# Kernel optimization log

Measured on AMD Instinct MI355X. Metric: run time of the kernel, lower is better.

The kernel has to match this reference:

```python
import jax, jax.numpy as jnp
import numpy as np

N_NODES = 50000
IN_DIM = 256
LATENT = 128
HIDDEN = 2 * LATENT  # 256


def _xavier(key, fan_in, fan_out):
    # matches nn.init.xavier_uniform_ on a [out, in] weight; we store as [in, out]
    limit = float(np.sqrt(6.0 / (fan_in + fan_out)))
    return jax.random.uniform(key, (fan_in, fan_out), jnp.float32, -limit, limit)


def setup_inputs() -> dict:
    key = jax.random.key(0)
    ks = jax.random.split(key, 8)
    x = jax.random.normal(ks[0], (N_NODES, IN_DIM), jnp.float32)
    edge_index = jax.random.randint(ks[1], (2, 800000), 0, N_NODES, jnp.int64)
    W1 = _xavier(ks[2], IN_DIM, HIDDEN)
    b1 = jnp.zeros((HIDDEN,), jnp.float32)
    Wmu = _xavier(ks[3], HIDDEN, LATENT)
    bmu = jnp.zeros((LATENT,), jnp.float32)
    Wlv = _xavier(ks[4], HIDDEN, LATENT)
    blv = jnp.zeros((LATENT,), jnp.float32)
    return {"x": x, "edge_index": edge_index, "W1": W1, "b1": b1,
            "Wmu": Wmu, "bmu": bmu, "Wlv": Wlv, "blv": blv}


def _gcn_layer(x, W, b, src, dst):
    # PyG GCNConv: h = x @ W; add self loops; symmetric norm; scatter-add; + bias
    h = x @ W  # [N, out]
    ones = jnp.ones(src.shape[0], x.dtype)
    deg = jax.ops.segment_sum(ones, dst, num_segments=N_NODES) + 1.0  # +1 for self loop
    dinv = jax.lax.rsqrt(deg)  # deg >= 1 always
    norm = dinv[src] * dinv[dst]  # [E]
    agg = jax.ops.segment_sum(h[src] * norm[:, None], dst, num_segments=N_NODES)
    agg = agg + h * (dinv * dinv)[:, None]  # self-loop contribution, norm_ii = 1/deg_i
    return agg + b


def reference(x, edge_index, W1, b1, Wmu, bmu, Wlv, blv):
    src, dst = edge_index[0], edge_index[1]
    z = _gcn_layer(x, W1, b1, src, dst)
    z = jax.nn.relu(z)
    # dropout in eval mode == identity
    mu = _gcn_layer(z, Wmu, bmu, src, dst)
    logvar = _gcn_layer(z, Wlv, blv, src, dst)
    return (mu, logvar)
```

## Files before the change

### kernel.cpp

```cpp
#include <hip/hip_runtime.h>

#define N_NODES 50000
#define E_EDGES 800000
#define D 256
#define L 128
#define CAP 64

typedef __attribute__((ext_vector_type(8))) short bf16x8;
typedef __attribute__((ext_vector_type(4))) float f32x4;

__device__ __forceinline__ float bf2f(unsigned short u) {
    union { unsigned int i; float f; } v; v.i = ((unsigned int)u) << 16; return v.f;
}
__device__ __forceinline__ unsigned short f2bf(float f) {
    union { float f; unsigned int i; } v; v.f = f;
    unsigned int r = v.i + 0x7fffu + ((v.i >> 16) & 1u);
    return (unsigned short)(r >> 16);
}

__global__ __launch_bounds__(256) void fill_fixed(const int* __restrict__ src,
                                                  const int* __restrict__ dst,
                                                  int* __restrict__ cursor,
                                                  int* __restrict__ bucket) {
    int e = blockIdx.x * 256 + threadIdx.x;
    if (e >= E_EDGES) return;
    int d = dst[e];
    int pos = atomicAdd(&cursor[d], 1);
    if (pos < CAP) bucket[d * CAP + pos] = src[e];
}

__global__ __launch_bounds__(256) void dinv_fin(const int* __restrict__ cursor,
                                                float* __restrict__ dinv) {
    int i = blockIdx.x * 256 + threadIdx.x;
    if (i < N_NODES) dinv[i] = rsqrtf((float)cursor[i] + 1.0f);
}

__global__ __launch_bounds__(256) void setup(
    const float* __restrict__ W1, const float* __restrict__ Wmu,
    const float* __restrict__ Wlv, const float* __restrict__ bmu,
    const float* __restrict__ blv,
    unsigned short* __restrict__ W1h, unsigned short* __restrict__ W1l,
    unsigned short* __restrict__ Wch, unsigned short* __restrict__ Wcl,
    float* __restrict__ bcat, int* __restrict__ cursor) {
    int b = blockIdx.x, t = threadIdx.x;
    if (b < 256) {
        int n = b, k = t;
        float w = W1[k * 256 + n];
        unsigned short h = f2bf(w);
        W1h[n * 256 + k] = h;
        W1l[n * 256 + k] = f2bf(w - bf2f(h));
    } else if (b < 512) {
        int n = b - 256, k = t;
        float w = (n < 128) ? Wmu[k * 128 + n] : Wlv[k * 128 + (n - 128)];
        unsigned short h = f2bf(w);
        Wch[n * 256 + k] = h;
        Wcl[n * 256 + k] = f2bf(w - bf2f(h));
        if (b == 256) bcat[t] = (t < 128) ? bmu[t] : blv[t - 128];
    } else {
        int i = (b - 512) * 256 + t;
        if (i < N_NODES) cursor[i] = 0;
    }
}

__global__ __launch_bounds__(256, 2) void gemm_mfma(
    const float* __restrict__ A,
    const unsigned short* __restrict__ Bth, const unsigned short* __restrict__ Btl,
    unsigned short* __restrict__ Hout, int M)
{
    __shared__ unsigned short Ash[128 * 32];
    __shared__ unsigned short Asl[128 * 32];
    __shared__ unsigned short Bsh[256 * 32];
    __shared__ unsigned short Bsl[256 * 32];
    const int t = threadIdx.x;
    const int lane = t & 63, wave = t >> 6;
    const int m_ = lane & 15, q = lane >> 4;
    const int wr = wave >> 1, wc = wave & 1;
    const int row0 = blockIdx.x * 128;
    const int sr = t >> 2;
    const int sc = t & 3;

    f32x4 acc[4][8];
    const f32x4 zf = {0.f, 0.f, 0.f, 0.f};
#pragma unroll
    for (int rs = 0; rs < 4; ++rs)
#pragma unroll
        for (int nt = 0; nt < 8; ++nt) acc[rs][nt] = zf;

    for (int ks = 0; ks < 8; ++ks) {
        const int k0 = ks * 32;
        bf16x8 gbh[4], gbl[4];
#pragma unroll
        for (int i = 0; i < 4; ++i) {
            int n = sr + i * 64;
            gbh[i] = *(const bf16x8*)(Bth + n * 256 + k0 + sc * 8);
            gbl[i] = *(const bf16x8*)(Btl + n * 256 + k0 + sc * 8);
        }
        float4 ga0[2], ga1[2];
#pragma unroll
        for (int p = 0; p < 2; ++p) {
            int r = row0 + p * 64 + sr; if (r >= M) r = M - 1;
            const float* Xp = A + (size_t)r * 256 + k0 + sc * 8;
            ga0[p] = *(const float4*)Xp;
            ga1[p] = *(const float4*)(Xp + 4);
        }
        __syncthreads();
#pragma unroll
        for (int p = 0; p < 2; ++p) {
            int lr = p * 64 + sr;
            int cc = (sc ^ ((lr >> 1) & 3)) * 8;
            float af[8] = {ga0[p].x, ga0[p].y, ga0[p].z, ga0[p].w,
                           ga1[p].x, ga1[p].y, ga1[p].z, ga1[p].w};
            bf16x8 h, l;
#pragma unroll
            for (int j = 0; j < 8; ++j) {
                unsigned short hh = f2bf(af[j]);
                h[j] = (short)hh;
                l[j] = (short)f2bf(af[j] - bf2f(hh));
            }
            *(bf16x8*)&Ash[lr * 32 + cc] = h;
            *(bf16x8*)&Asl[lr * 32 + cc] = l;
        }
#pragma unroll
        for (int i = 0; i < 4; ++i) {
            int n = sr + i * 64;
            int cc = (sc ^ ((n >> 1) & 3)) * 8;
            *(bf16x8*)&Bsh[n * 32 + cc] = gbh[i];
            *(bf16x8*)&Bsl[n * 32 + cc] = gbl[i];
        }
        __syncthreads();
        bf16x8 ah[4], al[4];
#pragma unroll
        for (int rs = 0; rs < 4; ++rs) {
            int r = wr * 64 + rs * 16 + m_;
            int cc = (q ^ ((r >> 1) & 3)) * 8;
            ah[rs] = *(const bf16x8*)&Ash[r * 32 + cc];
            al[rs] = *(const bf16x8*)&Asl[r * 32 + cc];
        }
#pragma unroll
        for (int nt = 0; nt < 8; ++nt) {
            int n = wc * 128 + nt * 16 + m_;
            int cr = (q ^ ((n >> 1) & 3)) * 8;
            bf16x8 bh = *(const bf16x8*)&Bsh[n * 32 + cr];
            bf16x8 bl = *(const bf16x8*)&Bsl[n * 32 + cr];
#pragma unroll
            for (int rs = 0; rs < 4; ++rs) {
                acc[rs][nt] = __builtin_amdgcn_mfma_f32_16x16x32_bf16(ah[rs], bh, acc[rs][nt], 0, 0, 0);
                acc[rs][nt] = __builtin_amdgcn_mfma_f32_16x16x32_bf16(ah[rs], bl, acc[rs][nt], 0, 0, 0);
                acc[rs][nt] = __builtin_amdgcn_mfma_f32_16x16x32_bf16(al[rs], bh, acc[rs][nt], 0, 0, 0);
            }
        }
    }
#pragma unroll
    for (int rs = 0; rs < 4; ++rs) {
        int rbase = row0 + wr * 64 + rs * 16 + q * 4;
#pragma unroll
        for (int rr = 0; rr < 4; ++rr) {
            int grow = rbase + rr;
            if (grow >= M) continue;
#pragma unroll
            for (int nt = 0; nt < 8; ++nt) {
                int gcol = wc * 128 + nt * 16 + m_;
                Hout[(size_t)grow * 256 + gcol] = f2bf(acc[rs][nt][rr]);
            }
        }
    }
}

__global__ __launch_bounds__(256, 2) void gemm_bf16(
    const unsigned short* __restrict__ A,
    const unsigned short* __restrict__ Bth, const unsigned short* __restrict__ Btl,
    unsigned short* __restrict__ Tout, int M)
{
    __shared__ unsigned short Ash[128 * 32];
    __shared__ unsigned short Bsh[256 * 32];
    __shared__ unsigned short Bsl[256 * 32];
    const int t = threadIdx.x;
    const int lane = t & 63, wave = t >> 6;
    const int m_ = lane & 15, q = lane >> 4;
    const int wr = wave >> 1, wc = wave & 1;
    const int row0 = blockIdx.x * 128;
    const int sr = t >> 2;
    const int sc = t & 3;

    f32x4 acc[4][8];
    const f32x4 zf = {0.f, 0.f, 0.f, 0.f};
#pragma unroll
    for (int rs = 0; rs < 4; ++rs)
#pragma unroll
        for (int nt = 0; nt < 8; ++nt) acc[rs][nt] = zf;

    for (int ks = 0; ks < 8; ++ks) {
        const int k0 = ks * 32;
        bf16x8 gbh[4], gbl[4];
#pragma unroll
        for (int i = 0; i < 4; ++i) {
            int n = sr + i * 64;
            gbh[i] = *(const bf16x8*)(Bth + n * 256 + k0 + sc * 8);
            gbl[i] = *(const bf16x8*)(Btl + n * 256 + k0 + sc * 8);
        }
        bf16x8 gav[2];
#pragma unroll
        for (int p = 0; p < 2; ++p) {
            int r = row0 + p * 64 + sr; if (r >= M) r = M - 1;
            gav[p] = *(const bf16x8*)(A + (size_t)r * 256 + k0 + sc * 8);
        }
        __syncthreads();
#pragma unroll
        for (int p = 0; p < 2; ++p) {
            int lr = p * 64 + sr;
            int cc = (sc ^ ((lr >> 1) & 3)) * 8;
            *(bf16x8*)&Ash[lr * 32 + cc] = gav[p];
        }
#pragma unroll
        for (int i = 0; i < 4; ++i) {
            int n = sr + i * 64;
            int cc = (sc ^ ((n >> 1) & 3)) * 8;
            *(bf16x8*)&Bsh[n * 32 + cc] = gbh[i];
            *(bf16x8*)&Bsl[n * 32 + cc] = gbl[i];
        }
        __syncthreads();
        bf16x8 ah[4];
#pragma unroll
        for (int rs = 0; rs < 4; ++rs) {
            int r = wr * 64 + rs * 16 + m_;
            int cc = (q ^ ((r >> 1) & 3)) * 8;
            ah[rs] = *(const bf16x8*)&Ash[r * 32 + cc];
        }
#pragma unroll
        for (int nt = 0; nt < 8; ++nt) {
            int n = wc * 128 + nt * 16 + m_;
            int cr = (q ^ ((n >> 1) & 3)) * 8;
            bf16x8 bh = *(const bf16x8*)&Bsh[n * 32 + cr];
            bf16x8 bl = *(const bf16x8*)&Bsl[n * 32 + cr];
#pragma unroll
            for (int rs = 0; rs < 4; ++rs) {
                acc[rs][nt] = __builtin_amdgcn_mfma_f32_16x16x32_bf16(ah[rs], bh, acc[rs][nt], 0, 0, 0);
                acc[rs][nt] = __builtin_amdgcn_mfma_f32_16x16x32_bf16(ah[rs], bl, acc[rs][nt], 0, 0, 0);
            }
        }
    }
#pragma unroll
    for (int rs = 0; rs < 4; ++rs) {
        int rbase = row0 + wr * 64 + rs * 16 + q * 4;
#pragma unroll
        for (int rr = 0; rr < 4; ++rr) {
            int grow = rbase + rr;
            if (grow >= M) continue;
#pragma unroll
            for (int nt = 0; nt < 8; ++nt) {
                int gcol = wc * 128 + nt * 16 + m_;
                Tout[(size_t)grow * 256 + gcol] = f2bf(acc[rs][nt][rr]);
            }
        }
    }
}

__global__ __launch_bounds__(256) void gather_pre(
    const unsigned short* __restrict__ Hs,
    const int* __restrict__ bucket, const int* __restrict__ cnt_,
    const float* __restrict__ dinv, const float* __restrict__ bias,
    unsigned short* __restrict__ OutZ,
    float* __restrict__ mu, float* __restrict__ lv, int mode)
{
    const int lane = threadIdx.x & 63;
    const int hl = lane & 31;
    const int bb = lane & 32;
    const int node = blockIdx.x * 8 + (threadIdx.x >> 5);
    const int col = hl * 8;
    int cnt = cnt_[node]; if (cnt > CAP) cnt = CAP;
    float dn = dinv[node];

    int   s0r = 0, s1r = 0;
    float w0r = 0.f, w1r = 0.f;
    if (hl < cnt)      { s0r = bucket[node * CAP + hl];      w0r = dinv[s0r] * dn; }
    if (hl + 32 < cnt) { s1r = bucket[node * CAP + 32 + hl]; w1r = dinv[s1r] * dn; }

    float sl = dn * dn;
    bf16x8 hv = *(const bf16x8*)(Hs + (size_t)node * D + col);
    float a[8];
#pragma unroll
    for (int p = 0; p < 8; ++p) a[p] = bf2f((unsigned short)hv[p]) * sl;

    const int cnt0 = cnt < 32 ? cnt : 32;
    int j = 0;
    for (; j + 3 < cnt0; j += 4) {
        int t0 = __shfl(s0r, bb + j,     64), t1 = __shfl(s0r, bb + j + 1, 64);
        int t2 = __shfl(s0r, bb + j + 2, 64), t3 = __shfl(s0r, bb + j + 3, 64);
        float w0 = __shfl(w0r, bb + j,     64), w1 = __shfl(w0r, bb + j + 1, 64);
        float w2 = __shfl(w0r, bb + j + 2, 64), w3 = __shfl(w0r, bb + j + 3, 64);
        bf16x8 u0 = *(const bf16x8*)(Hs + (size_t)t0 * D + col);
        bf16x8 u1 = *(const bf16x8*)(Hs + (size_t)t1 * D + col);
        bf16x8 u2 = *(const bf16x8*)(Hs + (size_t)t2 * D + col);
        bf16x8 u3 = *(const bf16x8*)(Hs + (size_t)t3 * D + col);
#pragma unroll
        for (int p = 0; p < 8; ++p) a[p] = fmaf(bf2f((unsigned short)u0[p]), w0, a[p]);
#pragma unroll
        for (int p = 0; p < 8; ++p) a[p] = fmaf(bf2f((unsigned short)u1[p]), w1, a[p]);
#pragma unroll
        for (int p = 0; p < 8; ++p) a[p] = fmaf(bf2f((unsigned short)u2[p]), w2, a[p]);
#pragma unroll
        for (int p = 0; p < 8; ++p) a[p] = fmaf(bf2f((unsigned short)u3[p]), w3, a[p]);
    }
    for (; j < cnt0; ++j) {
        int   t0 = __shfl(s0r, bb + j, 64);
        float w0 = __shfl(w0r, bb + j, 64);
        bf16x8 u0 = *(const bf16x8*)(Hs + (size_t)t0 * D + col);
#pragma unroll
        for (int p = 0; p < 8; ++p) a[p] = fmaf(bf2f((unsigned short)u0[p]), w0, a[p]);
    }
    if (cnt > 32) {
        for (int j2 = 0; j2 < cnt - 32; ++j2) {
            int   t0 = __shfl(s1r, bb + j2, 64);
            float w0 = __shfl(w1r, bb + j2, 64);
            bf16x8 u0 = *(const bf16x8*)(Hs + (size_t)t0 * D + col);
#pragma unroll
            for (int p = 0; p < 8; ++p) a[p] = fmaf(bf2f((unsigned short)u0[p]), w0, a[p]);
        }
    }

    float4 b0 = *(const float4*)(bias + col);
    float4 b1 = *(const float4*)(bias + col + 4);
    float bf[8] = {b0.x, b0.y, b0.z, b0.w, b1.x, b1.y, b1.z, b1.w};
    if (mode == 0) {
        bf16x8 o;
#pragma unroll
        for (int p = 0; p < 8; ++p) o[p] = (short)f2bf(fmaxf(a[p] + bf[p], 0.f));
        *(bf16x8*)(OutZ + (size_t)node * D + col) = o;
    } else {
        float4 o0, o1;
        o0.x = a[0] + bf[0]; o0.y = a[1] + bf[1];
        o0.z = a[2] + bf[2]; o0.w = a[3] + bf[3];
        o1.x = a[4] + bf[4]; o1.y = a[5] + bf[5];
        o1.z = a[6] + bf[6]; o1.w = a[7] + bf[7];
        float* Op = (col < 128) ? (mu + (size_t)node * L + col)
                                : (lv + (size_t)node * L + (col - 128));
        *(float4*)Op = o0;
        *(float4*)(Op + 4) = o1;
    }
}

extern "C" void kernel_launch(void* const* d_in, const int* in_sizes, int n_in,
                              void* d_out, int out_size, void* d_ws, size_t ws_size,
                              hipStream_t stream) {
    const float* x   = (const float*)d_in[0];
    const int*   ei  = (const int*)d_in[1];
    const float* W1  = (const float*)d_in[2];
    const float* b1  = (const float*)d_in[3];
    const float* Wmu = (const float*)d_in[4];
    const float* bmu = (const float*)d_in[5];
    const float* Wlv = (const float*)d_in[6];
    const float* blv = (const float*)d_in[7];
    const int* src = ei;
    const int* dst = ei + E_EDGES;

    const size_t NF = (size_t)N_NODES * D;
    unsigned short* Hb = (unsigned short*)d_ws;
    unsigned short* Z  = Hb + NF;
    unsigned short* T  = Z + NF;
    unsigned short* W1h = T + NF;
    unsigned short* W1l = W1h + 65536;
    unsigned short* Wch = W1l + 65536;
    unsigned short* Wcl = Wch + 65536;
    float* bcat = (float*)(Wcl + 65536);
    float* dinv = bcat + 256;
    int* cursor = (int*)(dinv + N_NODES);
    int* bucket = cursor + N_NODES;
    float* mu = (float*)d_out;
    float* lv = mu + (size_t)N_NODES * L;

    setup<<<512 + (N_NODES + 255) / 256, 256, 0, stream>>>(
        W1, Wmu, Wlv, bmu, blv, W1h, W1l, Wch, Wcl, bcat, cursor);
    fill_fixed<<<(E_EDGES + 255) / 256, 256, 0, stream>>>(src, dst, cursor, bucket);
    dinv_fin<<<(N_NODES + 255) / 256, 256, 0, stream>>>(cursor, dinv);

    const int gemm_blocks = (N_NODES + 127) / 128;
    const int gat_blocks  = N_NODES / 8;
    gemm_mfma<<<gemm_blocks, 256, 0, stream>>>(x, W1h, W1l, Hb, N_NODES);
    gather_pre<<<gat_blocks, 256, 0, stream>>>(Hb, bucket, cursor, dinv, b1,
                                               Z, nullptr, nullptr, 0);
    gemm_bf16<<<gemm_blocks, 256, 0, stream>>>(Z, Wch, Wcl, T, N_NODES);
    gather_pre<<<gat_blocks, 256, 0, stream>>>(T, bucket, cursor, dinv, bcat,
                                               nullptr, mu, lv, 1);
}
```

Baseline: 315.2 us.

## Halve GEMM row tile, prefetch next K slice, compute dinv inline in gather

Both GEMM kernels now use 64-row tiles instead of 128, with fewer accumulators and a launch bound of 3 blocks per CU. They also register-prefetch the next K slice of A and B while the current slice runs on MFMA. The dinv_fin kernel and its buffer are removed, and gather_pre computes rsqrt of degree+1 from the cursor counts on the fly. The aim is higher occupancy, better overlap of global loads with compute, and one fewer launch. The cost is more reloading of B per row, redundant rsqrt work in the gathers, and extra register pressure from the prefetch buffers.

```diff
diff --git a/kernel.cpp b/kernel.cpp
--- a/kernel.cpp
+++ b/kernel.cpp
@@ -27,12 +27,6 @@
     int d = dst[e];
     int pos = atomicAdd(&cursor[d], 1);
     if (pos < CAP) bucket[d * CAP + pos] = src[e];
-}
-
-__global__ __launch_bounds__(256) void dinv_fin(const int* __restrict__ cursor,
-                                                float* __restrict__ dinv) {
-    int i = blockIdx.x * 256 + threadIdx.x;
-    if (i < N_NODES) dinv[i] = rsqrtf((float)cursor[i] + 1.0f);
 }
 
 __global__ __launch_bounds__(256) void setup(
@@ -62,54 +56,49 @@
     }
 }
 
-__global__ __launch_bounds__(256, 2) void gemm_mfma(
+__global__ __launch_bounds__(256, 3) void gemm_mfma(
     const float* __restrict__ A,
     const unsigned short* __restrict__ Bth, const unsigned short* __restrict__ Btl,
     unsigned short* __restrict__ Hout, int M)
 {
-    __shared__ unsigned short Ash[128 * 32];
-    __shared__ unsigned short Asl[128 * 32];
+    __shared__ unsigned short Ash[64 * 32];
+    __shared__ unsigned short Asl[64 * 32];
     __shared__ unsigned short Bsh[256 * 32];
     __shared__ unsigned short Bsl[256 * 32];
     const int t = threadIdx.x;
     const int lane = t & 63, wave = t >> 6;
     const int m_ = lane & 15, q = lane >> 4;
     const int wr = wave >> 1, wc = wave & 1;
-    const int row0 = blockIdx.x * 128;
+    const int row0 = blockIdx.x * 64;
     const int sr = t >> 2;
     const int sc = t & 3;
 
-    f32x4 acc[4][8];
+    int rA = row0 + sr; if (rA >= M) rA = M - 1;
+    const float* Ap = A + (size_t)rA * 256;
+
+    f32x4 acc[2][8];
     const f32x4 zf = {0.f, 0.f, 0.f, 0.f};
 #pragma unroll
-    for (int rs = 0; rs < 4; ++rs)
+    for (int rs = 0; rs < 2; ++rs)
 #pragma unroll
         for (int nt = 0; nt < 8; ++nt) acc[rs][nt] = zf;
 
+    bf16x8 gbh[4], gbl[4];
+    float4 ga0, ga1;
+#pragma unroll
+    for (int i = 0; i < 4; ++i) {
+        int n = sr + i * 64;
+        gbh[i] = *(const bf16x8*)(Bth + n * 256 + sc * 8);
+        gbl[i] = *(const bf16x8*)(Btl + n * 256 + sc * 8);
+    }
+    ga0 = *(const float4*)(Ap + sc * 8);
+    ga1 = *(const float4*)(Ap + sc * 8 + 4);
+
     for (int ks = 0; ks < 8; ++ks) {
-        const int k0 = ks * 32;
-        bf16x8 gbh[4], gbl[4];
-#pragma unroll
-        for (int i = 0; i < 4; ++i) {
-            int n = sr + i * 64;
-            gbh[i] = *(const bf16x8*)(Bth + n * 256 + k0 + sc * 8);
-            gbl[i] = *(const bf16x8*)(Btl + n * 256 + k0 + sc * 8);
-        }
-        float4 ga0[2], ga1[2];
-#pragma unroll
-        for (int p = 0; p < 2; ++p) {
-            int r = row0 + p * 64 + sr; if (r >= M) r = M - 1;
-            const float* Xp = A + (size_t)r * 256 + k0 + sc * 8;
-            ga0[p] = *(const float4*)Xp;
-            ga1[p] = *(const float4*)(Xp + 4);
-        }
         __syncthreads();
-#pragma unroll
-        for (int p = 0; p < 2; ++p) {
-            int lr = p * 64 + sr;
-            int cc = (sc ^ ((lr >> 1) & 3)) * 8;
-            float af[8] = {ga0[p].x, ga0[p].y, ga0[p].z, ga0[p].w,
-                           ga1[p].x, ga1[p].y, ga1[p].z, ga1[p].w};
+        {
+            int cc = (sc ^ ((sr >> 1) & 3)) * 8;
+            float af[8] = {ga0.x, ga0.y, ga0.z, ga0.w, ga1.x, ga1.y, ga1.z, ga1.w};
             bf16x8 h, l;
 #pragma unroll
             for (int j = 0; j < 8; ++j) {
@@ -117,8 +106,8 @@
                 h[j] = (short)hh;
                 l[j] = (short)f2bf(af[j] - bf2f(hh));
             }
-            *(bf16x8*)&Ash[lr * 32 + cc] = h;
-            *(bf16x8*)&Asl[lr * 32 + cc] = l;
+            *(bf16x8*)&Ash[sr * 32 + cc] = h;
+            *(bf16x8*)&Asl[sr * 32 + cc] = l;
         }
 #pragma unroll
         for (int i = 0; i < 4; ++i) {
@@ -128,10 +117,21 @@
             *(bf16x8*)&Bsl[n * 32 + cc] = gbl[i];
         }
         __syncthreads();
-        bf16x8 ah[4], al[4];
-#pragma unroll
-        for (int rs = 0; rs < 4; ++rs) {
-            int r = wr * 64 + rs * 16 + m_;
+        if (ks < 7) {
+            const int k1 = (ks + 1) * 32;
+#pragma unroll
+            for (int i = 0; i < 4; ++i) {
+                int n = sr + i * 64;
+                gbh[i] = *(const bf16x8*)(Bth + n * 256 + k1 + sc * 8);
+                gbl[i] = *(const bf16x8*)(Btl + n * 256 + k1 + sc * 8);
+            }
+            ga0 = *(const float4*)(Ap + k1 + sc * 8);
+            ga1 = *(const float4*)(Ap + k1 + sc * 8 + 4);
+        }
+        bf16x8 ah[2], al[2];
+#pragma unroll
+        for (int rs = 0; rs < 2; ++rs) {
+            int r = wr * 32 + rs * 16 + m_;
             int cc = (q ^ ((r >> 1) & 3)) * 8;
             ah[rs] = *(const bf16x8*)&Ash[r * 32 + cc];
             al[rs] = *(const bf16x8*)&Asl[r * 32 + cc];
@@ -143,7 +143,7 @@
             bf16x8 bh = *(const bf16x8*)&Bsh[n * 32 + cr];
             bf16x8 bl = *(const bf16x8*)&Bsl[n * 32 + cr];
 #pragma unroll
-            for (int rs = 0; rs < 4; ++rs) {
+            for (int rs = 0; rs < 2; ++rs) {
                 acc[rs][nt] = __builtin_amdgcn_mfma_f32_16x16x32_bf16(ah[rs], bh, acc[rs][nt], 0, 0, 0);
                 acc[rs][nt] = __builtin_amdgcn_mfma_f32_16x16x32_bf16(ah[rs], bl, acc[rs][nt], 0, 0, 0);
                 acc[rs][nt] = __builtin_amdgcn_mfma_f32_16x16x32_bf16(al[rs], bh, acc[rs][nt], 0, 0, 0);
@@ -151,8 +151,8 @@
         }
     }
 #pragma unroll
-    for (int rs = 0; rs < 4; ++rs) {
-        int rbase = row0 + wr * 64 + rs * 16 + q * 4;
+    for (int rs = 0; rs < 2; ++rs) {
+        int rbase = row0 + wr * 32 + rs * 16 + q * 4;
 #pragma unroll
         for (int rr = 0; rr < 4; ++rr) {
             int grow = rbase + rr;
@@ -166,50 +166,46 @@
     }
 }
 
-__global__ __launch_bounds__(256, 2) void gemm_bf16(
+__global__ __launch_bounds__(256, 3) void gemm_bf16(
     const unsigned short* __restrict__ A,
     const unsigned short* __restrict__ Bth, const unsigned short* __restrict__ Btl,
     unsigned short* __restrict__ Tout, int M)
 {
-    __shared__ unsigned short Ash[128 * 32];
+    __shared__ unsigned short Ash[64 * 32];
     __shared__ unsigned short Bsh[256 * 32];
     __shared__ unsigned short Bsl[256 * 32];
     const int t = threadIdx.x;
     const int lane = t & 63, wave = t >> 6;
     const int m_ = lane & 15, q = lane >> 4;
     const int wr = wave >> 1, wc = wave & 1;
-    const int row0 = blockIdx.x * 128;
+    const int row0 = blockIdx.x * 64;
     const int sr = t >> 2;
     const int sc = t & 3;
 
-    f32x4 acc[4][8];
+    int rA = row0 + sr; if (rA >= M) rA = M - 1;
+    const unsigned short* Ap = A + (size_t)rA * 256;
+
+    f32x4 acc[2][8];
     const f32x4 zf = {0.f, 0.f, 0.f, 0.f};
 #pragma unroll
-    for (int rs = 0; rs < 4; ++rs)
+    for (int rs = 0; rs < 2; ++rs)
 #pragma unroll
         for (int nt = 0; nt < 8; ++nt) acc[rs][nt] = zf;
 
+    bf16x8 gbh[4], gbl[4], gav;
+#pragma unroll
+    for (int i = 0; i < 4; ++i) {
+        int n = sr + i * 64;
+        gbh[i] = *(const bf16x8*)(Bth + n * 256 + sc * 8);
+        gbl[i] = *(const bf16x8*)(Btl + n * 256 + sc * 8);
+    }
+    gav = *(const bf16x8*)(Ap + sc * 8);
+
     for (int ks = 0; ks < 8; ++ks) {
-        const int k0 = ks * 32;
-        bf16x8 gbh[4], gbl[4];
-#pragma unroll
-        for (int i = 0; i < 4; ++i) {
-            int n = sr + i * 64;
-            gbh[i] = *(const bf16x8*)(Bth + n * 256 + k0 + sc * 8);
-            gbl[i] = *(const bf16x8*)(Btl + n * 256 + k0 + sc * 8);
-        }
-        bf16x8 gav[2];
-#pragma unroll
-        for (int p = 0; p < 2; ++p) {
-            int r = row0 + p * 64 + sr; if (r >= M) r = M - 1;
-            gav[p] = *(const bf16x8*)(A + (size_t)r * 256 + k0 + sc * 8);
-        }
         __syncthreads();
-#pragma unroll
-        for (int p = 0; p < 2; ++p) {
-            int lr = p * 64 + sr;
-            int cc = (sc ^ ((lr >> 1) & 3)) * 8;
-            *(bf16x8*)&Ash[lr * 32 + cc] = gav[p];
+        {
+            int cc = (sc ^ ((sr >> 1) & 3)) * 8;
+            *(bf16x8*)&Ash[sr * 32 + cc] = gav;
         }
 #pragma unroll
         for (int i = 0; i < 4; ++i) {
@@ -219,10 +215,20 @@
             *(bf16x8*)&Bsl[n * 32 + cc] = gbl[i];
         }
         __syncthreads();
-        bf16x8 ah[4];
-#pragma unroll
-        for (int rs = 0; rs < 4; ++rs) {
-            int r = wr * 64 + rs * 16 + m_;
+        if (ks < 7) {
+            const int k1 = (ks + 1) * 32;
+#pragma unroll
+            for (int i = 0; i < 4; ++i) {
+                int n = sr + i * 64;
+                gbh[i] = *(const bf16x8*)(Bth + n * 256 + k1 + sc * 8);
+                gbl[i] = *(const bf16x8*)(Btl + n * 256 + k1 + sc * 8);
+            }
+            gav = *(const bf16x8*)(Ap + k1 + sc * 8);
+        }
+        bf16x8 ah[2];
+#pragma unroll
+        for (int rs = 0; rs < 2; ++rs) {
+            int r = wr * 32 + rs * 16 + m_;
             int cc = (q ^ ((r >> 1) & 3)) * 8;
             ah[rs] = *(const bf16x8*)&Ash[r * 32 + cc];
         }
@@ -233,15 +239,15 @@
             bf16x8 bh = *(const bf16x8*)&Bsh[n * 32 + cr];
             bf16x8 bl = *(const bf16x8*)&Bsl[n * 32 + cr];
 #pragma unroll
-            for (int rs = 0; rs < 4; ++rs) {
+            for (int rs = 0; rs < 2; ++rs) {
                 acc[rs][nt] = __builtin_amdgcn_mfma_f32_16x16x32_bf16(ah[rs], bh, acc[rs][nt], 0, 0, 0);
                 acc[rs][nt] = __builtin_amdgcn_mfma_f32_16x16x32_bf16(ah[rs], bl, acc[rs][nt], 0, 0, 0);
             }
         }
     }
 #pragma unroll
-    for (int rs = 0; rs < 4; ++rs) {
-        int rbase = row0 + wr * 64 + rs * 16 + q * 4;
+    for (int rs = 0; rs < 2; ++rs) {
+        int rbase = row0 + wr * 32 + rs * 16 + q * 4;
 #pragma unroll
         for (int rr = 0; rr < 4; ++rr) {
             int grow = rbase + rr;
@@ -258,7 +264,7 @@
 __global__ __launch_bounds__(256) void gather_pre(
     const unsigned short* __restrict__ Hs,
     const int* __restrict__ bucket, const int* __restrict__ cnt_,
-    const float* __restrict__ dinv, const float* __restrict__ bias,
+    const float* __restrict__ bias,
     unsigned short* __restrict__ OutZ,
     float* __restrict__ mu, float* __restrict__ lv, int mode)
 {
@@ -267,13 +273,20 @@
     const int bb = lane & 32;
     const int node = blockIdx.x * 8 + (threadIdx.x >> 5);
     const int col = hl * 8;
-    int cnt = cnt_[node]; if (cnt > CAP) cnt = CAP;
-    float dn = dinv[node];
+    int raw = cnt_[node];
+    float dn = rsqrtf((float)raw + 1.0f);
+    int cnt = raw > CAP ? CAP : raw;
 
     int   s0r = 0, s1r = 0;
     float w0r = 0.f, w1r = 0.f;
-    if (hl < cnt)      { s0r = bucket[node * CAP + hl];      w0r = dinv[s0r] * dn; }
-    if (hl + 32 < cnt) { s1r = bucket[node * CAP + 32 + hl]; w1r = dinv[s1r] * dn; }
+    if (hl < cnt) {
+        s0r = bucket[node * CAP + hl];
+        w0r = rsqrtf((float)cnt_[s0r] + 1.0f) * dn;
+    }
+    if (hl + 32 < cnt) {
+        s1r = bucket[node * CAP + 32 + hl];
+        w1r = rsqrtf((float)cnt_[s1r] + 1.0f) * dn;
+    }
 
     float sl = dn * dn;
     bf16x8 hv = *(const bf16x8*)(Hs + (size_t)node * D + col);
@@ -362,8 +375,7 @@
     unsigned short* Wch = W1l + 65536;
     unsigned short* Wcl = Wch + 65536;
     float* bcat = (float*)(Wcl + 65536);
-    float* dinv = bcat + 256;
-    int* cursor = (int*)(dinv + N_NODES);
+    int* cursor = (int*)(bcat + 256);
     int* bucket = cursor + N_NODES;
     float* mu = (float*)d_out;
     float* lv = mu + (size_t)N_NODES * L;
@@ -371,14 +383,13 @@
     setup<<<512 + (N_NODES + 255) / 256, 256, 0, stream>>>(
         W1, Wmu, Wlv, bmu, blv, W1h, W1l, Wch, Wcl, bcat, cursor);
     fill_fixed<<<(E_EDGES + 255) / 256, 256, 0, stream>>>(src, dst, cursor, bucket);
-    dinv_fin<<<(N_NODES + 255) / 256, 256, 0, stream>>>(cursor, dinv);
-
-    const int gemm_blocks = (N_NODES + 127) / 128;
+
+    const int gemm_blocks = (N_NODES + 63) / 64;
     const int gat_blocks  = N_NODES / 8;
     gemm_mfma<<<gemm_blocks, 256, 0, stream>>>(x, W1h, W1l, Hb, N_NODES);
-    gather_pre<<<gat_blocks, 256, 0, stream>>>(Hb, bucket, cursor, dinv, b1,
+    gather_pre<<<gat_blocks, 256, 0, stream>>>(Hb, bucket, cursor, b1,
                                                Z, nullptr, nullptr, 0);
     gemm_bf16<<<gemm_blocks, 256, 0, stream>>>(Z, Wch, Wcl, T, N_NODES);
-    gather_pre<<<gat_blocks, 256, 0, stream>>>(T, bucket, cursor, dinv, bcat,
+    gather_pre<<<gat_blocks, 256, 0, stream>>>(T, bucket, cursor, bcat,
                                                nullptr, mu, lv, 1);
 }
```

Result: slower. 327.8 us (+4.0%).
